# Optimization experiments

Measured on AMD Instinct MI355X. Metric: run time of the kernel, lower is better.

## Reference

```python
import jax, jax.numpy as jnp
import numpy as np

N_NODES = 100000
N_EDGES = 600000
D_IN = 128
D_OUT = 128


def setup_inputs() -> dict:
    key = jax.random.key(0)
    k1, k2, k3 = jax.random.split(key, 3)
    x = jax.random.normal(k1, (N_NODES, D_IN), dtype=jnp.float32)
    edge_index = jax.random.randint(k2, (2, N_EDGES), 0, N_NODES, dtype=jnp.int32)
    W = jax.random.normal(k3, (D_OUT, D_IN), dtype=jnp.float32) * 0.02
    b = jnp.zeros((D_OUT,), dtype=jnp.float32)
    return {"x": x, "edge_index": edge_index, "W": W, "b": b}


def reference(x, edge_index, W, b):
    # x: [N, D], edge_index: [2, E]
    n = x.shape[0]
    src = edge_index[0]
    dst = edge_index[1]
    # gather + elementwise abs diff: [E, D]
    msg = jnp.abs(x[src] - x[dst])
    # scatter-mean with out=x.clone(): sum includes the initial x values,
    # count is the number of scattered edges per node. Self-loops add a zero
    # message and +1 to the count, so counts = out_degree + 1 >= 1.
    sums = x + jax.ops.segment_sum(msg, src, num_segments=n)
    counts = jax.ops.segment_sum(jnp.ones_like(src, dtype=x.dtype), src, num_segments=n) + 1.0
    out = sums / counts[:, None]
    # Linear
    return out @ W.T + b
```

## Files before the change

kernel.cpp:

```cpp
#include <hip/hip_runtime.h>

#define D 128
#define CHB 8
#define CHSZ 256
#define TILE 2048
#define CAPCH 1856
#define SCAN_N 512
#define CAPQ 960
#define PADW 136
#define MAXDEG 32

typedef __attribute__((ext_vector_type(8))) short bf16x8;
typedef __attribute__((ext_vector_type(4))) short bf16x4;
typedef __attribute__((ext_vector_type(4))) unsigned short u16x4;
typedef __attribute__((ext_vector_type(4))) float f32x4;

__device__ inline short f2bf(float f) {
    unsigned u = __float_as_uint(f);
    unsigned r = (u + 0x7fff + ((u >> 16) & 1)) >> 16;
    return (short)r;
}
__device__ inline bf16x8 pack8(float4 a, float4 b) {
    bf16x8 r;
    r[0] = f2bf(a.x); r[1] = f2bf(a.y); r[2] = f2bf(a.z); r[3] = f2bf(a.w);
    r[4] = f2bf(b.x); r[5] = f2bf(b.y); r[6] = f2bf(b.z); r[7] = f2bf(b.w);
    return r;
}
__device__ inline float bf2f(unsigned short h) {
    return __uint_as_float(((unsigned)h) << 16);
}

__global__ __launch_bounds__(256) void zero_ints(int* __restrict__ g, int n) {
    int i = blockIdx.x * 256 + threadIdx.x;
    if (i < n) g[i] = 0;
}

__global__ __launch_bounds__(256) void prep3(const float* __restrict__ x,
                                             unsigned short* __restrict__ xh,
                                             const int* __restrict__ ei,
                                             int* __restrict__ gcur,
                                             int2* __restrict__ part,
                                             const float* __restrict__ Wg,
                                             bf16x8* __restrict__ Wpk,
                                             int N, int E, int NT, int NCH) {
    __shared__ int hist[SCAN_N];
    __shared__ int pref[SCAN_N];
    __shared__ int gbase[SCAN_N];
    __shared__ int2 sedge[TILE];
    int t = threadIdx.x;
    if ((int)blockIdx.x < NT) {
        int e0 = blockIdx.x * TILE;
        int cntT = E - e0; if (cntT > TILE) cntT = TILE;
        for (int i = t; i < SCAN_N; i += 256) hist[i] = 0;
        __syncthreads();

        int src[8], dst[8], rk[8];
        int base8 = e0 + t * 8;
        if (base8 + 8 <= E) {
            int4 s0 = *(const int4*)(ei + base8);
            int4 s1 = *(const int4*)(ei + base8 + 4);
            int4 d0 = *(const int4*)(ei + E + base8);
            int4 d1 = *(const int4*)(ei + E + base8 + 4);
            src[0]=s0.x; src[1]=s0.y; src[2]=s0.z; src[3]=s0.w;
            src[4]=s1.x; src[5]=s1.y; src[6]=s1.z; src[7]=s1.w;
            dst[0]=d0.x; dst[1]=d0.y; dst[2]=d0.z; dst[3]=d0.w;
            dst[4]=d1.x; dst[5]=d1.y; dst[6]=d1.z; dst[7]=d1.w;
        } else {
#pragma unroll
            for (int k = 0; k < 8; ++k) {
                int g = base8 + k;
                src[k] = (g < E) ? ei[g] : 0;
                dst[k] = (g < E) ? ei[E + g] : 0;
            }
        }
#pragma unroll
        for (int k = 0; k < 8; ++k) {
            rk[k] = (t * 8 + k < cntT) ? atomicAdd(&hist[src[k] >> CHB], 1) : -1;
        }
        __syncthreads();
        if (t == 0) {
            int acc = 0;
            for (int i = 0; i < SCAN_N; ++i) { pref[i] = acc; acc += hist[i]; }
        }
        __syncthreads();
        for (int c = t; c < NCH; c += 256)
            gbase[c] = hist[c] ? atomicAdd(&gcur[c], hist[c]) : 0;
#pragma unroll
        for (int k = 0; k < 8; ++k)
            if (rk[k] >= 0)
                sedge[pref[src[k] >> CHB] + rk[k]] = make_int2(src[k], dst[k]);
        __syncthreads();
        for (int i = t; i < cntT; i += 256) {
            int2 e = sedge[i];
            int c = e.x >> CHB;
            int slot = gbase[c] + (i - pref[c]);
            if (slot < CAPCH) part[(size_t)c * CAPCH + slot] = e;
        }
    } else if ((int)blockIdx.x == NT) {
        for (int i = t; i < 2048; i += 256) {
            int f = i >> 6, l = i & 63;
            int n16 = f >> 2, kk = f & 3;
            int c = n16 * 16 + (l & 15);
            int k0 = kk * 32 + (l >> 4) * 8;
            float4 p0 = *(const float4*)(Wg + c * D + k0);
            float4 p1 = *(const float4*)(Wg + c * D + k0 + 4);
            Wpk[i] = pack8(p0, p1);
        }
    } else {
        long idx = (long)(blockIdx.x - NT - 1) * 256 + t;
        long total = (long)N * D / 8;
        if (idx < total) {
            const float4* xp = (const float4*)x;
            float4 p0 = xp[idx * 2];
            float4 p1 = xp[idx * 2 + 1];
            ((bf16x8*)xh)[idx] = pack8(p0, p1);
        }
    }
}

__global__ __launch_bounds__(256) void aggmm(const unsigned short* __restrict__ xh,
                                             const int* __restrict__ gcur,
                                             const int2* __restrict__ part,
                                             const bf16x8* __restrict__ Wpk,
                                             const float* __restrict__ bvec,
                                             float* __restrict__ out, int N) {
    __shared__ int nh[64];
    __shared__ int off[65];
    __shared__ int adj[CAPQ];
    __shared__ __align__(16) short tile[64 * PADW];
    int t = threadIdx.x;
    int ch = blockIdx.x >> 2;
    int sub = blockIdx.x & 3;
    int nbase = (ch << CHB) + sub * 64;
    int cnt = gcur[ch]; if (cnt > CAPCH) cnt = CAPCH;
    if (t < 64) nh[t] = 0;
    __syncthreads();

    int2 e2[8]; int rk2[8];
#pragma unroll
    for (int ii = 0; ii < 8; ++ii) {
        int i = ii * 256 + t;
        rk2[ii] = -1;
        if (i < cnt) {
            int2 e = part[(size_t)ch * CAPCH + i];
            int rl = e.x & (CHSZ - 1);
            if ((rl >> 6) == sub) {
                e2[ii] = e;
                rk2[ii] = atomicAdd(&nh[rl & 63], 1);
            }
        }
    }
    __syncthreads();
    if (t == 0) {
        int acc = 0;
        for (int i = 0; i < 64; ++i) { off[i] = acc; acc += nh[i]; }
        off[64] = acc;
    }
    __syncthreads();
#pragma unroll
    for (int ii = 0; ii < 8; ++ii)
        if (rk2[ii] >= 0) {
            int idx = off[e2[ii].x & 63] + rk2[ii];
            if (idx < CAPQ) adj[idx] = e2[ii].y;
        }
    __syncthreads();

    int team = t >> 5, lane = t & 31;
    for (int rl = team; rl < 64; rl += 8) {
        int r = nbase + rl;
        bf16x4* lp = (bf16x4*)&tile[rl * PADW + lane * 4];
        if (r >= N) { bf16x4 z = {0, 0, 0, 0}; *lp = z; continue; }
        int deg = nh[rl];
        int ab = off[rl];
        int dg = deg;
        if (ab + dg > CAPQ) dg = CAPQ - ab;
        if (dg < 0) dg = 0;
        u16x4 ah = *(const u16x4*)(xh + (size_t)r * D + lane * 4);
        float4 a;
        a.x = bf2f(ah[0]); a.y = bf2f(ah[1]); a.z = bf2f(ah[2]); a.w = bf2f(ah[3]);
        float4 a0 = a;
        float4 a1 = {0, 0, 0, 0}, a2 = {0, 0, 0, 0}, a3 = {0, 0, 0, 0};
        for (int f = 0; f < dg; f += 4) {
            int d0 = adj[ab + f];
            int d1 = (f + 1 < dg) ? adj[ab + f + 1] : r;
            int d2 = (f + 2 < dg) ? adj[ab + f + 2] : r;
            int d3 = (f + 3 < dg) ? adj[ab + f + 3] : r;
            u16x4 v0 = *(const u16x4*)(xh + (size_t)d0 * D + lane * 4);
            u16x4 v1 = *(const u16x4*)(xh + (size_t)d1 * D + lane * 4);
            u16x4 v2 = *(const u16x4*)(xh + (size_t)d2 * D + lane * 4);
            u16x4 v3 = *(const u16x4*)(xh + (size_t)d3 * D + lane * 4);
            a0.x += fabsf(a.x - bf2f(v0[0])); a0.y += fabsf(a.y - bf2f(v0[1]));
            a0.z += fabsf(a.z - bf2f(v0[2])); a0.w += fabsf(a.w - bf2f(v0[3]));
            a1.x += fabsf(a.x - bf2f(v1[0])); a1.y += fabsf(a.y - bf2f(v1[1]));
            a1.z += fabsf(a.z - bf2f(v1[2])); a1.w += fabsf(a.w - bf2f(v1[3]));
            a2.x += fabsf(a.x - bf2f(v2[0])); a2.y += fabsf(a.y - bf2f(v2[1]));
            a2.z += fabsf(a.z - bf2f(v2[2])); a2.w += fabsf(a.w - bf2f(v2[3]));
            a3.x += fabsf(a.x - bf2f(v3[0])); a3.y += fabsf(a.y - bf2f(v3[1]));
            a3.z += fabsf(a.z - bf2f(v3[2])); a3.w += fabsf(a.w - bf2f(v3[3]));
        }
        float s = 1.0f / (float)(deg + 1);
        bf16x4 p;
        p[0] = f2bf(((a0.x + a1.x) + (a2.x + a3.x)) * s);
        p[1] = f2bf(((a0.y + a1.y) + (a2.y + a3.y)) * s);
        p[2] = f2bf(((a0.z + a1.z) + (a2.z + a3.z)) * s);
        p[3] = f2bf(((a0.w + a1.w) + (a2.w + a3.w)) * s);
        *lp = p;
    }

    __syncthreads();

    int w = t >> 6;
    int l = t & 63;
    int rw = w >> 1, cw = w & 1;
    int l15 = l & 15, lk8 = (l >> 4) * 8;

    bf16x8 Af[2][4];
#pragma unroll
    for (int m = 0; m < 2; ++m) {
        int row = rw * 32 + m * 16 + l15;
#pragma unroll
        for (int kk = 0; kk < 4; ++kk)
            Af[m][kk] = *(const bf16x8*)&tile[row * PADW + kk * 32 + lk8];
    }

    f32x4 acc[2][4] = {};
#pragma unroll
    for (int n = 0; n < 4; ++n) {
        int col16 = cw * 4 + n;
#pragma unroll
        for (int kk = 0; kk < 4; ++kk) {
            bf16x8 Bf = Wpk[(col16 * 4 + kk) * 64 + l];
            acc[0][n] = __builtin_amdgcn_mfma_f32_16x16x32_bf16(Af[0][kk], Bf, acc[0][n], 0, 0, 0);
            acc[1][n] = __builtin_amdgcn_mfma_f32_16x16x32_bf16(Af[1][kk], Bf, acc[1][n], 0, 0, 0);
        }
    }

#pragma unroll
    for (int m = 0; m < 2; ++m) {
        int r0 = nbase + rw * 32 + m * 16 + (l >> 4) * 4;
#pragma unroll
        for (int n = 0; n < 4; ++n) {
            int c = cw * 64 + n * 16 + l15;
            float bias = bvec[c];
#pragma unroll
            for (int j = 0; j < 4; ++j) {
                int r = r0 + j;
                if (r < N) out[(size_t)r * D + c] = acc[m][n][j] + bias;
            }
        }
    }
}

__global__ __launch_bounds__(256) void bucket_fb(const int* __restrict__ ei,
                                                 int* __restrict__ cnt,
                                                 int* __restrict__ bucket, int E) {
    int e = blockIdx.x * 256 + threadIdx.x;
    if (e >= E) return;
    int src = ei[e];
    int dst = ei[E + e];
    int pos = atomicAdd(&cnt[src], 1);
    if (pos < MAXDEG) bucket[src * MAXDEG + pos] = dst;
}

__global__ __launch_bounds__(256) void agg_f32(const float* __restrict__ x,
                                               const int* __restrict__ cnt,
                                               const int* __restrict__ bucket,
                                               float* __restrict__ y, int N) {
    int t = blockIdx.x * 256 + threadIdx.x;
    int team = t >> 5;
    int lane = t & 31;
    if (team >= N) return;
    int r = team;
    int deg = cnt[r];
    float4 a = ((const float4*)(x + (size_t)r * D))[lane];
    int m = deg < MAXDEG ? deg : MAXDEG;
    const int* bk = bucket + (size_t)r * MAXDEG;
    float4 a0 = a, a1 = {0,0,0,0}, a2 = {0,0,0,0}, a3 = {0,0,0,0};
    for (int j = 0; j < m; j += 4) {
        int4 d4 = *(const int4*)(bk + j);
        int d0 = d4.x;
        int d1 = (j + 1 < m) ? d4.y : r;
        int d2 = (j + 2 < m) ? d4.z : r;
        int d3 = (j + 3 < m) ? d4.w : r;
        float4 v0 = ((const float4*)(x + (size_t)d0 * D))[lane];
        float4 v1 = ((const float4*)(x + (size_t)d1 * D))[lane];
        float4 v2 = ((const float4*)(x + (size_t)d2 * D))[lane];
        float4 v3 = ((const float4*)(x + (size_t)d3 * D))[lane];
        a0.x += fabsf(a.x - v0.x); a0.y += fabsf(a.y - v0.y);
        a0.z += fabsf(a.z - v0.z); a0.w += fabsf(a.w - v0.w);
        a1.x += fabsf(a.x - v1.x); a1.y += fabsf(a.y - v1.y);
        a1.z += fabsf(a.z - v1.z); a1.w += fabsf(a.w - v1.w);
        a2.x += fabsf(a.x - v2.x); a2.y += fabsf(a.y - v2.y);
        a2.z += fabsf(a.z - v2.z); a2.w += fabsf(a.w - v2.w);
        a3.x += fabsf(a.x - v3.x); a3.y += fabsf(a.y - v3.y);
        a3.z += fabsf(a.z - v3.z); a3.w += fabsf(a.w - v3.w);
    }
    float s = 1.0f / (float)(deg + 1);
    float4 o;
    o.x = ((a0.x + a1.x) + (a2.x + a3.x)) * s;
    o.y = ((a0.y + a1.y) + (a2.y + a3.y)) * s;
    o.z = ((a0.z + a1.z) + (a2.z + a3.z)) * s;
    o.w = ((a0.w + a1.w) + (a2.w + a3.w)) * s;
    ((float4*)(y + (size_t)r * D))[lane] = o;
}

__global__ __launch_bounds__(256) void mfma_f32(const float* y,
                                                const float* __restrict__ W,
                                                const float* __restrict__ b,
                                                float* out, int N) {
    int w = threadIdx.x >> 6;
    int l = threadIdx.x & 63;
    int rw = w >> 1;
    int cw = w & 1;
    int l15 = l & 15;
    int lk8 = (l >> 4) * 8;
    bf16x8 Bf[4][4];
    float bias[4];
#pragma unroll
    for (int n = 0; n < 4; ++n) {
        int c = cw * 64 + n * 16 + l15;
        const float* wr = W + c * D;
        bias[n] = b[c];
#pragma unroll
        for (int kk = 0; kk < 4; ++kk) {
            float4 p0 = *(const float4*)(wr + kk * 32 + lk8);
            float4 p1 = *(const float4*)(wr + kk * 32 + lk8 + 4);
            Bf[n][kk] = pack8(p0, p1);
        }
    }
    int rowbase = blockIdx.x * 64 + rw * 32;
    bf16x8 Af[2][4];
#pragma unroll
    for (int m = 0; m < 2; ++m) {
        int r = rowbase + m * 16 + l15;
        int rc = r < N ? r : N - 1;
        const float* yr = y + (size_t)rc * D;
#pragma unroll
        for (int kk = 0; kk < 4; ++kk) {
            float4 p0 = *(const float4*)(yr + kk * 32 + lk8);
            float4 p1 = *(const float4*)(yr + kk * 32 + lk8 + 4);
            Af[m][kk] = pack8(p0, p1);
        }
    }
    f32x4 acc[2][4] = {};
#pragma unroll
    for (int m = 0; m < 2; ++m)
#pragma unroll
        for (int n = 0; n < 4; ++n)
#pragma unroll
            for (int kk = 0; kk < 4; ++kk)
                acc[m][n] = __builtin_amdgcn_mfma_f32_16x16x32_bf16(
                    Af[m][kk], Bf[n][kk], acc[m][n], 0, 0, 0);
#pragma unroll
    for (int m = 0; m < 2; ++m) {
        int r0 = rowbase + m * 16 + (l >> 4) * 4;
#pragma unroll
        for (int n = 0; n < 4; ++n) {
            int c = cw * 64 + n * 16 + l15;
#pragma unroll
            for (int j = 0; j < 4; ++j) {
                int r = r0 + j;
                if (r < N) out[(size_t)r * D + c] = acc[m][n][j] + bias[n];
            }
        }
    }
}

extern "C" void kernel_launch(void* const* d_in, const int* in_sizes, int n_in,
                              void* d_out, int out_size, void* d_ws, size_t ws_size,
                              hipStream_t stream) {
    const float* x  = (const float*)d_in[0];
    const int*   ei = (const int*)d_in[1];
    const float* W  = (const float*)d_in[2];
    const float* b  = (const float*)d_in[3];
    float* out = (float*)d_out;

    int N = in_sizes[0] / D;
    int E = in_sizes[1] / 2;

    int NCH = (N + CHSZ - 1) >> CHB;
    int NT  = (E + TILE - 1) / TILE;

    char* ws = (char*)d_ws;
    unsigned short* xh = (unsigned short*)ws;
    int2* part = (int2*)(ws + (size_t)N * D * 2);
    int* gcur = (int*)(part + (size_t)NCH * CAPCH);
    size_t wpo = (((size_t)((char*)(gcur + NCH) - ws)) + 255) & ~(size_t)255;
    bf16x8* Wpk = (bf16x8*)(ws + wpo);
    size_t need = wpo + 32768;

    bool ok = (ws_size >= need) && (NCH <= SCAN_N);

    if (ok) {
        zero_ints<<<(NCH + 255) / 256, 256, 0, stream>>>(gcur, NCH);
        long conv_threads = (long)N * D / 8;
        int cblocks = (int)((conv_threads + 255) / 256);
        prep3<<<NT + 1 + cblocks, 256, 0, stream>>>(x, xh, ei, gcur, part, W, Wpk,
                                                    N, E, NT, NCH);
        aggmm<<<NCH * 4, 256, 0, stream>>>(xh, gcur, part, Wpk, b, out, N);
    } else {
        int* cnt    = (int*)d_ws;
        int* bucket = cnt + N;
        int teams_per_block = 256 / 32;
        int ablocks = (N + teams_per_block - 1) / teams_per_block;
        zero_ints<<<(N + 255) / 256, 256, 0, stream>>>(cnt, N);
        bucket_fb<<<(E + 255) / 256, 256, 0, stream>>>(ei, cnt, bucket, E);
        agg_f32<<<ablocks, 256, 0, stream>>>(x, cnt, bucket, out, N);
        mfma_f32<<<(N + 63) / 64, 256, 0, stream>>>(out, W, b, out, N);
    }
}
```

Baseline: 82.82 us.

## Split aggmm blocks to 32 rows and unroll neighbor gather by eight

Each aggregation+matmul block now handles 32 rows instead of 64, launching twice as many blocks per chunk to raise parallelism and cut shared memory per block. The neighbor gather loop is unrolled to 8 independent loads with 8 accumulators to expose more memory-level parallelism. Edge records are re-read from global memory instead of held in registers, which lowers register pressure. The cost is that every block re-scans the full chunk's edge list, doubling that traffic, and each wave does fewer MFMAs per W fragment load.

```diff
diff --git a/kernel.cpp b/kernel.cpp
--- a/kernel.cpp
+++ b/kernel.cpp
@@ -6,7 +6,8 @@
 #define TILE 2048
 #define CAPCH 1856
 #define SCAN_N 512
-#define CAPQ 960
+#define ROWS 32
+#define CAPQ 512
 #define PADW 136
 #define MAXDEG 32
 
@@ -124,49 +125,48 @@
                                              const bf16x8* __restrict__ Wpk,
                                              const float* __restrict__ bvec,
                                              float* __restrict__ out, int N) {
-    __shared__ int nh[64];
-    __shared__ int off[65];
+    __shared__ int nh[ROWS];
+    __shared__ int off[ROWS + 1];
     __shared__ int adj[CAPQ];
-    __shared__ __align__(16) short tile[64 * PADW];
+    __shared__ __align__(16) short tile[ROWS * PADW];
     int t = threadIdx.x;
-    int ch = blockIdx.x >> 2;
-    int sub = blockIdx.x & 3;
-    int nbase = (ch << CHB) + sub * 64;
+    int ch = blockIdx.x >> 3;
+    int sub = blockIdx.x & 7;
+    int nbase = (ch << CHB) + sub * ROWS;
     int cnt = gcur[ch]; if (cnt > CAPCH) cnt = CAPCH;
-    if (t < 64) nh[t] = 0;
+    if (t < ROWS) nh[t] = 0;
     __syncthreads();
 
-    int2 e2[8]; int rk2[8];
+    const int2* pchunk = part + (size_t)ch * CAPCH;
+    int rk2[8];
 #pragma unroll
     for (int ii = 0; ii < 8; ++ii) {
         int i = ii * 256 + t;
         rk2[ii] = -1;
         if (i < cnt) {
-            int2 e = part[(size_t)ch * CAPCH + i];
+            int2 e = pchunk[i];
             int rl = e.x & (CHSZ - 1);
-            if ((rl >> 6) == sub) {
-                e2[ii] = e;
-                rk2[ii] = atomicAdd(&nh[rl & 63], 1);
-            }
+            if ((rl >> 5) == sub) rk2[ii] = atomicAdd(&nh[rl & (ROWS - 1)], 1);
         }
     }
     __syncthreads();
     if (t == 0) {
         int acc = 0;
-        for (int i = 0; i < 64; ++i) { off[i] = acc; acc += nh[i]; }
-        off[64] = acc;
+        for (int i = 0; i < ROWS; ++i) { off[i] = acc; acc += nh[i]; }
+        off[ROWS] = acc;
     }
     __syncthreads();
 #pragma unroll
     for (int ii = 0; ii < 8; ++ii)
         if (rk2[ii] >= 0) {
-            int idx = off[e2[ii].x & 63] + rk2[ii];
-            if (idx < CAPQ) adj[idx] = e2[ii].y;
+            int2 e = pchunk[ii * 256 + t];
+            int idx = off[e.x & (ROWS - 1)] + rk2[ii];
+            if (idx < CAPQ) adj[idx] = e.y;
         }
     __syncthreads();
 
     int team = t >> 5, lane = t & 31;
-    for (int rl = team; rl < 64; rl += 8) {
+    for (int rl = team; rl < ROWS; rl += 8) {
         int r = nbase + rl;
         bf16x4* lp = (bf16x4*)&tile[rl * PADW + lane * 4];
         if (r >= N) { bf16x4 z = {0, 0, 0, 0}; *lp = z; continue; }
@@ -178,32 +178,45 @@
         u16x4 ah = *(const u16x4*)(xh + (size_t)r * D + lane * 4);
         float4 a;
         a.x = bf2f(ah[0]); a.y = bf2f(ah[1]); a.z = bf2f(ah[2]); a.w = bf2f(ah[3]);
-        float4 a0 = a;
-        float4 a1 = {0, 0, 0, 0}, a2 = {0, 0, 0, 0}, a3 = {0, 0, 0, 0};
-        for (int f = 0; f < dg; f += 4) {
-            int d0 = adj[ab + f];
-            int d1 = (f + 1 < dg) ? adj[ab + f + 1] : r;
-            int d2 = (f + 2 < dg) ? adj[ab + f + 2] : r;
-            int d3 = (f + 3 < dg) ? adj[ab + f + 3] : r;
-            u16x4 v0 = *(const u16x4*)(xh + (size_t)d0 * D + lane * 4);
-            u16x4 v1 = *(const u16x4*)(xh + (size_t)d1 * D + lane * 4);
-            u16x4 v2 = *(const u16x4*)(xh + (size_t)d2 * D + lane * 4);
-            u16x4 v3 = *(const u16x4*)(xh + (size_t)d3 * D + lane * 4);
-            a0.x += fabsf(a.x - bf2f(v0[0])); a0.y += fabsf(a.y - bf2f(v0[1]));
-            a0.z += fabsf(a.z - bf2f(v0[2])); a0.w += fabsf(a.w - bf2f(v0[3]));
-            a1.x += fabsf(a.x - bf2f(v1[0])); a1.y += fabsf(a.y - bf2f(v1[1]));
-            a1.z += fabsf(a.z - bf2f(v1[2])); a1.w += fabsf(a.w - bf2f(v1[3]));
-            a2.x += fabsf(a.x - bf2f(v2[0])); a2.y += fabsf(a.y - bf2f(v2[1]));
-            a2.z += fabsf(a.z - bf2f(v2[2])); a2.w += fabsf(a.w - bf2f(v2[3]));
-            a3.x += fabsf(a.x - bf2f(v3[0])); a3.y += fabsf(a.y - bf2f(v3[1]));
-            a3.z += fabsf(a.z - bf2f(v3[2])); a3.w += fabsf(a.w - bf2f(v3[3]));
+        float4 s0 = a;
+        float4 s1 = {0,0,0,0}, s2 = {0,0,0,0}, s3 = {0,0,0,0};
+        float4 s4 = {0,0,0,0}, s5 = {0,0,0,0}, s6 = {0,0,0,0}, s7 = {0,0,0,0};
+        for (int f = 0; f < dg; f += 8) {
+            int dd[8];
+#pragma unroll
+            for (int q = 0; q < 8; ++q)
+                dd[q] = (f + q < dg) ? adj[ab + f + q] : r;
+            u16x4 v0 = *(const u16x4*)(xh + (size_t)dd[0] * D + lane * 4);
+            u16x4 v1 = *(const u16x4*)(xh + (size_t)dd[1] * D + lane * 4);
+            u16x4 v2 = *(const u16x4*)(xh + (size_t)dd[2] * D + lane * 4);
+            u16x4 v3 = *(const u16x4*)(xh + (size_t)dd[3] * D + lane * 4);
+            u16x4 v4 = *(const u16x4*)(xh + (size_t)dd[4] * D + lane * 4);
+            u16x4 v5 = *(const u16x4*)(xh + (size_t)dd[5] * D + lane * 4);
+            u16x4 v6 = *(const u16x4*)(xh + (size_t)dd[6] * D + lane * 4);
+            u16x4 v7 = *(const u16x4*)(xh + (size_t)dd[7] * D + lane * 4);
+            s0.x += fabsf(a.x - bf2f(v0[0])); s0.y += fabsf(a.y - bf2f(v0[1]));
+            s0.z += fabsf(a.z - bf2f(v0[2])); s0.w += fabsf(a.w - bf2f(v0[3]));
+            s1.x += fabsf(a.x - bf2f(v1[0])); s1.y += fabsf(a.y - bf2f(v1[1]));
+            s1.z += fabsf(a.z - bf2f(v1[2])); s1.w += fabsf(a.w - bf2f(v1[3]));
+            s2.x += fabsf(a.x - bf2f(v2[0])); s2.y += fabsf(a.y - bf2f(v2[1]));
+            s2.z += fabsf(a.z - bf2f(v2[2])); s2.w += fabsf(a.w - bf2f(v2[3]));
+            s3.x += fabsf(a.x - bf2f(v3[0])); s3.y += fabsf(a.y - bf2f(v3[1]));
+            s3.z += fabsf(a.z - bf2f(v3[2])); s3.w += fabsf(a.w - bf2f(v3[3]));
+            s4.x += fabsf(a.x - bf2f(v4[0])); s4.y += fabsf(a.y - bf2f(v4[1]));
+            s4.z += fabsf(a.z - bf2f(v4[2])); s4.w += fabsf(a.w - bf2f(v4[3]));
+            s5.x += fabsf(a.x - bf2f(v5[0])); s5.y += fabsf(a.y - bf2f(v5[1]));
+            s5.z += fabsf(a.z - bf2f(v5[2])); s5.w += fabsf(a.w - bf2f(v5[3]));
+            s6.x += fabsf(a.x - bf2f(v6[0])); s6.y += fabsf(a.y - bf2f(v6[1]));
+            s6.z += fabsf(a.z - bf2f(v6[2])); s6.w += fabsf(a.w - bf2f(v6[3]));
+            s7.x += fabsf(a.x - bf2f(v7[0])); s7.y += fabsf(a.y - bf2f(v7[1]));
+            s7.z += fabsf(a.z - bf2f(v7[2])); s7.w += fabsf(a.w - bf2f(v7[3]));
         }
         float s = 1.0f / (float)(deg + 1);
         bf16x4 p;
-        p[0] = f2bf(((a0.x + a1.x) + (a2.x + a3.x)) * s);
-        p[1] = f2bf(((a0.y + a1.y) + (a2.y + a3.y)) * s);
-        p[2] = f2bf(((a0.z + a1.z) + (a2.z + a3.z)) * s);
-        p[3] = f2bf(((a0.w + a1.w) + (a2.w + a3.w)) * s);
+        p[0] = f2bf((((s0.x + s1.x) + (s2.x + s3.x)) + ((s4.x + s5.x) + (s6.x + s7.x))) * s);
+        p[1] = f2bf((((s0.y + s1.y) + (s2.y + s3.y)) + ((s4.y + s5.y) + (s6.y + s7.y))) * s);
+        p[2] = f2bf((((s0.z + s1.z) + (s2.z + s3.z)) + ((s4.z + s5.z) + (s6.z + s7.z))) * s);
+        p[3] = f2bf((((s0.w + s1.w) + (s2.w + s3.w)) + ((s4.w + s5.w) + (s6.w + s7.w))) * s);
         *lp = p;
     }
 
@@ -214,39 +227,32 @@
     int rw = w >> 1, cw = w & 1;
     int l15 = l & 15, lk8 = (l >> 4) * 8;
 
-    bf16x8 Af[2][4];
-#pragma unroll
-    for (int m = 0; m < 2; ++m) {
-        int row = rw * 32 + m * 16 + l15;
-#pragma unroll
-        for (int kk = 0; kk < 4; ++kk)
-            Af[m][kk] = *(const bf16x8*)&tile[row * PADW + kk * 32 + lk8];
-    }
-
-    f32x4 acc[2][4] = {};
+    bf16x8 Af[4];
+    int row = rw * 16 + l15;
+#pragma unroll
+    for (int kk = 0; kk < 4; ++kk)
+        Af[kk] = *(const bf16x8*)&tile[row * PADW + kk * 32 + lk8];
+
+    f32x4 acc[4] = {};
 #pragma unroll
     for (int n = 0; n < 4; ++n) {
         int col16 = cw * 4 + n;
 #pragma unroll
         for (int kk = 0; kk < 4; ++kk) {
             bf16x8 Bf = Wpk[(col16 * 4 + kk) * 64 + l];
-            acc[0][n] = __builtin_amdgcn_mfma_f32_16x16x32_bf16(Af[0][kk], Bf, acc[0][n], 0, 0, 0);
-            acc[1][n] = __builtin_amdgcn_mfma_f32_16x16x32_bf16(Af[1][kk], Bf, acc[1][n], 0, 0, 0);
-        }
-    }
-
-#pragma unroll
-    for (int m = 0; m < 2; ++m) {
-        int r0 = nbase + rw * 32 + m * 16 + (l >> 4) * 4;
-#pragma unroll
-        for (int n = 0; n < 4; ++n) {
-            int c = cw * 64 + n * 16 + l15;
-            float bias = bvec[c];
-#pragma unroll
-            for (int j = 0; j < 4; ++j) {
-                int r = r0 + j;
-                if (r < N) out[(size_t)r * D + c] = acc[m][n][j] + bias;
-            }
+            acc[n] = __builtin_amdgcn_mfma_f32_16x16x32_bf16(Af[kk], Bf, acc[n], 0, 0, 0);
+        }
+    }
+
+    int r0 = nbase + rw * 16 + (l >> 4) * 4;
+#pragma unroll
+    for (int n = 0; n < 4; ++n) {
+        int c = cw * 64 + n * 16 + l15;
+        float bias = bvec[c];
+#pragma unroll
+        for (int j = 0; j < 4; ++j) {
+            int r = r0 + j;
+            if (r < N) out[(size_t)r * D + c] = acc[n][j] + bias;
         }
     }
 }
@@ -397,7 +403,7 @@
         int cblocks = (int)((conv_threads + 255) / 256);
         prep3<<<NT + 1 + cblocks, 256, 0, stream>>>(x, xh, ei, gcur, part, W, Wpk,
                                                     N, E, NT, NCH);
-        aggmm<<<NCH * 4, 256, 0, stream>>>(xh, gcur, part, Wpk, b, out, N);
+        aggmm<<<NCH * 8, 256, 0, stream>>>(xh, gcur, part, Wpk, b, out, N);
     } else {
         int* cnt    = (int*)d_ws;
         int* bucket = cnt + N;
```

New measurement: 96.72 us. 16.8% more time.
